# Kernel tuning notes

Measured on AMD Instinct MI355X. Metric: run time of the kernel, lower is better.

## Reference

```python
import jax, jax.numpy as jnp
import numpy as np

C_CURV = 1.0  # hyperbolic curvature (init kwarg c)
EPS = 1e-7


def _to_ball(v, max_norm=0.8):
    # rescale rows to lie strictly inside the unit Poincare ball
    n = jnp.linalg.norm(v, axis=-1, keepdims=True)
    return v * (max_norm / (n + 1.0))


def setup_inputs() -> dict:
    key = jax.random.key(0)
    k1, k2 = jax.random.split(key)
    B, C, D = 32768, 2048, 512
    z_mix = _to_ball(jax.random.normal(k1, (B, D), dtype=jnp.float32))
    prototypes = _to_ball(jax.random.normal(k2, (C, D), dtype=jnp.float32))
    repel_margin = jnp.float32(2.0)
    return {"z_mix": z_mix, "prototypes": prototypes, "repel_margin": repel_margin}


def dist_matrix(x, y, c):
    # Poincare-ball pairwise distance (arccosh form):
    # d(x,y) = arccosh(1 + 2c||x-y||^2 / ((1-c||x||^2)(1-c||y||^2))) / sqrt(c)
    x2 = jnp.sum(x * x, axis=-1)            # (B,)
    y2 = jnp.sum(y * y, axis=-1)            # (C,)
    xy = jnp.einsum('bd,cd->bc', x, y)      # (B, C)
    sqdist = jnp.maximum(x2[:, None] + y2[None, :] - 2.0 * xy, 0.0)
    denom = (1.0 - c * x2)[:, None] * (1.0 - c * y2)[None, :]
    arg = 1.0 + 2.0 * c * sqdist / jnp.maximum(denom, EPS)
    return jnp.arccosh(jnp.maximum(arg, 1.0 + EPS)) / jnp.sqrt(c)


def reference(z_mix, prototypes, repel_margin):
    dist2proto = dist_matrix(z_mix, prototypes, C_CURV)   # (B, C)
    min_dist = jnp.min(dist2proto, axis=1)                # (B,)
    return jnp.mean(jax.nn.relu(repel_margin - min_dist))
```

## Files before the change

kernel.cpp:

```cpp
#include <hip/hip_runtime.h>
#include <stdint.h>

#define EPS_F 1e-7f

typedef float f32x4 __attribute__((ext_vector_type(4)));

union A8 { uint2 u2; long l; };

__device__ __forceinline__ unsigned cvt4(float a, float b, float c, float d) {
  int v = __builtin_amdgcn_cvt_pk_fp8_f32(a, b, 0, false);
  return (unsigned)__builtin_amdgcn_cvt_pk_fp8_f32(c, d, v, true);
}

__global__ __launch_bounds__(256) void prep_kernel(
    const float* __restrict__ protos, uint8_t* __restrict__ wsB,
    float* __restrict__ y2a, float* __restrict__ rya,
    float* __restrict__ out) {
  const int lane = threadIdx.x & 63;
  const int w    = threadIdx.x >> 6;
  const int kp2  = lane >> 2, q = lane & 3;
  const int sl0  = 8 * kp2 + q;
  const int sl1  = sl0 + 4;
#pragma unroll
  for (int i = 0; i < 4; ++i) {
    int c = (blockIdx.x * 4 + w) * 4 + i;
    const float4* p = (const float4*)(protos + (size_t)c * 512 + lane * 8);
    float4 f0 = p[0], f1 = p[1];
    float s = f0.x*f0.x + f0.y*f0.y + f0.z*f0.z + f0.w*f0.w
            + f1.x*f1.x + f1.y*f1.y + f1.z*f1.z + f1.w*f1.w;
#pragma unroll
    for (int off = 32; off > 0; off >>= 1) s += __shfl_xor(s, off, 64);
    if (lane == 0) { y2a[c] = s; rya[c] = 1.f / (1.f - s); }
    unsigned ux = cvt4(f0.x, f0.y, f0.z, f0.w);
    unsigned uy = cvt4(f1.x, f1.y, f1.z, f1.w);
    uint4 ch;
    ch.x = __shfl((int)ux, sl0, 64);
    ch.y = __shfl((int)uy, sl0, 64);
    ch.z = __shfl((int)ux, sl1, 64);
    ch.w = __shfl((int)uy, sl1, 64);
    if (lane < 32) {
      int g = c >> 4, cl = c & 15;
      ((uint4*)wsB)[((size_t)g * 8 + kp2) * 64 + q * 16 + cl] = ch;
    }
  }
  if (blockIdx.x == 0 && threadIdx.x == 0) out[0] = 0.f;
}

__global__ __launch_bounds__(256, 2) void gemm_min_kernel(
    const float* __restrict__ z, const uint8_t* __restrict__ wsB,
    const float* __restrict__ y2a, const float* __restrict__ rya,
    const float* __restrict__ marg, float* __restrict__ out) {
  __shared__ uint8_t As[32 * 1024];
  __shared__ float x2s[64];
  __shared__ float rxs[64];
  __shared__ float minbuf[64][4];

  const int tid  = threadIdx.x;
  const int lane = tid & 63;
  const int w    = tid >> 6;
  const int q    = lane >> 4;
  const int l15  = lane & 15;
  const size_t rowbase = (size_t)blockIdx.x * 64;

  {
    const float* rp0 = z + (rowbase + w * 16 + l15) * 512;
    float s = 0.f;
#pragma unroll
    for (int j = 0; j < 8; ++j) {
      const float* rp = rp0 + j * 64 + q * 8;
      float4 a0 = ((const float4*)rp)[0];
      float4 a1 = ((const float4*)rp)[1];
      float4 b0 = ((const float4*)(rp + 32))[0];
      float4 b1 = ((const float4*)(rp + 32))[1];
      s += a0.x*a0.x + a0.y*a0.y + a0.z*a0.z + a0.w*a0.w
         + a1.x*a1.x + a1.y*a1.y + a1.z*a1.z + a1.w*a1.w
         + b0.x*b0.x + b0.y*b0.y + b0.z*b0.z + b0.w*b0.w
         + b1.x*b1.x + b1.y*b1.y + b1.z*b1.z + b1.w*b1.w;
      uint4 ch;
      ch.x = cvt4(a0.x, a0.y, a0.z, a0.w);
      ch.y = cvt4(a1.x, a1.y, a1.z, a1.w);
      ch.z = cvt4(b0.x, b0.y, b0.z, b0.w);
      ch.w = cvt4(b1.x, b1.y, b1.z, b1.w);
      ((uint4*)As)[(j * 4 + w) * 64 + lane] = ch;
    }
    s += __shfl_xor(s, 16, 64);
    s += __shfl_xor(s, 32, 64);
    if (lane < 16) { x2s[w * 16 + lane] = s; rxs[w * 16 + lane] = 1.f / (1.f - s); }
  }
  __syncthreads();

  float x2r[4][4];
#pragma unroll
  for (int rf = 0; rf < 4; ++rf) {
    float4 x4 = *(const float4*)&x2s[rf * 16 + q * 4];
    x2r[rf][0] = x4.x; x2r[rf][1] = x4.y; x2r[rf][2] = x4.z; x2r[rf][3] = x4.w;
  }

  const uint4* Ap = (const uint4*)As;
  const uint4* Bg = (const uint4*)wsB;

  uint4 B0w[4], B1w[4];
#pragma unroll
  for (int i = 0; i < 4; ++i) {
    B0w[i] = Bg[(size_t)(w * 256 + i) * 64 + lane];
    B1w[i] = Bg[(size_t)(w * 256 + 8 + i) * 64 + lane];
  }

  float tmin[4][4];
#pragma unroll
  for (int rf = 0; rf < 4; ++rf)
#pragma unroll
    for (int r = 0; r < 4; ++r) tmin[rf][r] = 3.4e38f;

  const float* y2p = y2a + w * 512 + l15;
  const float* ryp = rya + w * 512 + l15;

#pragma clang loop unroll(disable)
  for (int s = 0; s < 16; ++s) {
    f32x4 acc[4][2];
#pragma unroll
    for (int rf = 0; rf < 4; ++rf) {
      f32x4 z4 = {0.f, 0.f, 0.f, 0.f};
      acc[rf][0] = z4; acc[rf][1] = z4;
    }
    float y2v0 = y2p[s * 32],      ryv0 = ryp[s * 32];
    float y2v1 = y2p[s * 32 + 16], ryv1 = ryp[s * 32 + 16];

#pragma unroll
    for (int kp2 = 0; kp2 < 8; ++kp2) {
      uint4 bu0 = B0w[kp2 & 3];
      uint4 bu1 = B1w[kp2 & 3];
      {
        int ip = s * 8 + kp2 + 4;
        int sp = ip >> 3, kq = ip & 7;
        size_t c0 = (size_t)(w * 256 + sp * 16 + kq) * 64 + lane;
        B0w[kp2 & 3] = Bg[c0];
        B1w[kp2 & 3] = Bg[c0 + 8 * 64];
      }
      A8 b0lo, b0hi, b1lo, b1hi;
      b0lo.u2 = make_uint2(bu0.x, bu0.y); b0hi.u2 = make_uint2(bu0.z, bu0.w);
      b1lo.u2 = make_uint2(bu1.x, bu1.y); b1hi.u2 = make_uint2(bu1.z, bu1.w);
#pragma unroll
      for (int rf = 0; rf < 4; ++rf) {
        uint4 av = Ap[(kp2 * 4 + rf) * 64 + lane];
        A8 alo, ahi;
        alo.u2 = make_uint2(av.x, av.y);
        ahi.u2 = make_uint2(av.z, av.w);
        acc[rf][0] = __builtin_amdgcn_mfma_f32_16x16x32_fp8_fp8(
            alo.l, b0lo.l, acc[rf][0], 0, 0, 0);
        acc[rf][1] = __builtin_amdgcn_mfma_f32_16x16x32_fp8_fp8(
            alo.l, b1lo.l, acc[rf][1], 0, 0, 0);
        acc[rf][0] = __builtin_amdgcn_mfma_f32_16x16x32_fp8_fp8(
            ahi.l, b0hi.l, acc[rf][0], 0, 0, 0);
        acc[rf][1] = __builtin_amdgcn_mfma_f32_16x16x32_fp8_fp8(
            ahi.l, b1hi.l, acc[rf][1], 0, 0, 0);
      }
    }

#pragma unroll
    for (int rf = 0; rf < 4; ++rf) {
#pragma unroll
      for (int r = 0; r < 4; ++r) {
        float xv = x2r[rf][r];
        float u0 = fmaxf(fmaf(-2.f, acc[rf][0][r], xv + y2v0), 0.f) * ryv0;
        float u1 = fmaxf(fmaf(-2.f, acc[rf][1][r], xv + y2v1), 0.f) * ryv1;
        tmin[rf][r] = fminf(tmin[rf][r], fminf(u0, u1));
      }
    }
  }

#pragma unroll
  for (int rf = 0; rf < 4; ++rf) {
#pragma unroll
    for (int r = 0; r < 4; ++r) {
      float v = tmin[rf][r];
      v = fminf(v, __shfl_xor(v, 1, 64));
      v = fminf(v, __shfl_xor(v, 2, 64));
      v = fminf(v, __shfl_xor(v, 4, 64));
      v = fminf(v, __shfl_xor(v, 8, 64));
      if (l15 == 0) minbuf[rf * 16 + q * 4 + r][w] = v;
    }
  }
  __syncthreads();

  if (w == 0) {
    float m = fminf(fminf(minbuf[lane][0], minbuf[lane][1]),
                    fminf(minbuf[lane][2], minbuf[lane][3]));
    float t = m * rxs[lane];
    float arg = fmaxf(fmaf(2.f, t, 1.f), 1.f + EPS_F);
    float contrib = fmaxf(marg[0] - acoshf(arg), 0.f);
#pragma unroll
    for (int off = 32; off > 0; off >>= 1) contrib += __shfl_xor(contrib, off, 64);
    if (lane == 0) atomicAdd(out, contrib * (1.0f / 32768.f));
  }
}

extern "C" void kernel_launch(void* const* d_in, const int* in_sizes, int n_in,
                              void* d_out, int out_size, void* d_ws, size_t ws_size,
                              hipStream_t stream) {
  const float* z      = (const float*)d_in[0];
  const float* protos = (const float*)d_in[1];
  const float* marg   = (const float*)d_in[2];
  float* out = (float*)d_out;
  uint8_t* wsB = (uint8_t*)d_ws;
  float* y2a = (float*)((char*)d_ws + (1 << 20) + 192 * 1024);
  float* rya = y2a + 2048;

  prep_kernel<<<128, 256, 0, stream>>>(protos, wsB, y2a, rya, out);
  gemm_min_kernel<<<512, 256, 0, stream>>>(z, wsB, y2a, rya, marg, out);
}
```

Measured before the change: 155.9 us.

## Split prototype dimension across two blocks per row tile with atomic row-min

The GEMM-min kernel now launches 1024 blocks, with each row tile split into two halves of the prototype range. Partial row minima are merged with atomicMin on the float bits, and a new finish kernel applies acosh, the margin and the mean. The prep kernel is re-gridded to one prototype per wave and also initialises the row-min buffer. This doubles the grid to improve occupancy and tail balance on many CUs, at the cost of converting every z row tile to fp8 twice, an extra launch and extra global traffic.

```diff
diff --git a/kernel.cpp b/kernel.cpp
--- a/kernel.cpp
+++ b/kernel.cpp
@@ -15,44 +15,42 @@
 __global__ __launch_bounds__(256) void prep_kernel(
     const float* __restrict__ protos, uint8_t* __restrict__ wsB,
     float* __restrict__ y2a, float* __restrict__ rya,
-    float* __restrict__ out) {
+    unsigned* __restrict__ rowminU, float* __restrict__ out) {
   const int lane = threadIdx.x & 63;
   const int w    = threadIdx.x >> 6;
   const int kp2  = lane >> 2, q = lane & 3;
   const int sl0  = 8 * kp2 + q;
   const int sl1  = sl0 + 4;
-#pragma unroll
-  for (int i = 0; i < 4; ++i) {
-    int c = (blockIdx.x * 4 + w) * 4 + i;
-    const float4* p = (const float4*)(protos + (size_t)c * 512 + lane * 8);
-    float4 f0 = p[0], f1 = p[1];
-    float s = f0.x*f0.x + f0.y*f0.y + f0.z*f0.z + f0.w*f0.w
-            + f1.x*f1.x + f1.y*f1.y + f1.z*f1.z + f1.w*f1.w;
-#pragma unroll
-    for (int off = 32; off > 0; off >>= 1) s += __shfl_xor(s, off, 64);
-    if (lane == 0) { y2a[c] = s; rya[c] = 1.f / (1.f - s); }
-    unsigned ux = cvt4(f0.x, f0.y, f0.z, f0.w);
-    unsigned uy = cvt4(f1.x, f1.y, f1.z, f1.w);
-    uint4 ch;
-    ch.x = __shfl((int)ux, sl0, 64);
-    ch.y = __shfl((int)uy, sl0, 64);
-    ch.z = __shfl((int)ux, sl1, 64);
-    ch.w = __shfl((int)uy, sl1, 64);
-    if (lane < 32) {
-      int g = c >> 4, cl = c & 15;
-      ((uint4*)wsB)[((size_t)g * 8 + kp2) * 64 + q * 16 + cl] = ch;
-    }
-  }
-  if (blockIdx.x == 0 && threadIdx.x == 0) out[0] = 0.f;
+  const int c = blockIdx.x * 4 + w;
+  const float4* p = (const float4*)(protos + (size_t)c * 512 + lane * 8);
+  float4 f0 = p[0], f1 = p[1];
+  float s = f0.x*f0.x + f0.y*f0.y + f0.z*f0.z + f0.w*f0.w
+          + f1.x*f1.x + f1.y*f1.y + f1.z*f1.z + f1.w*f1.w;
+#pragma unroll
+  for (int off = 32; off > 0; off >>= 1) s += __shfl_xor(s, off, 64);
+  if (lane == 0) { y2a[c] = s; rya[c] = 1.f / (1.f - s); }
+  unsigned ux = cvt4(f0.x, f0.y, f0.z, f0.w);
+  unsigned uy = cvt4(f1.x, f1.y, f1.z, f1.w);
+  uint4 ch;
+  ch.x = __shfl((int)ux, sl0, 64);
+  ch.y = __shfl((int)uy, sl0, 64);
+  ch.z = __shfl((int)ux, sl1, 64);
+  ch.w = __shfl((int)uy, sl1, 64);
+  if (lane < 32) {
+    int g = c >> 4, cl = c & 15;
+    ((uint4*)wsB)[((size_t)g * 8 + kp2) * 64 + q * 16 + cl] = ch;
+  }
+  int tidg = blockIdx.x * 256 + threadIdx.x;
+  if (tidg < 32768) rowminU[tidg] = 0x7F7FFFFFu;
+  if (tidg == 0) out[0] = 0.f;
 }
 
 __global__ __launch_bounds__(256, 2) void gemm_min_kernel(
     const float* __restrict__ z, const uint8_t* __restrict__ wsB,
     const float* __restrict__ y2a, const float* __restrict__ rya,
-    const float* __restrict__ marg, float* __restrict__ out) {
+    float* __restrict__ rxa, unsigned* __restrict__ rowminU) {
   __shared__ uint8_t As[32 * 1024];
   __shared__ float x2s[64];
-  __shared__ float rxs[64];
   __shared__ float minbuf[64][4];
 
   const int tid  = threadIdx.x;
@@ -60,7 +58,19 @@
   const int w    = tid >> 6;
   const int q    = lane >> 4;
   const int l15  = lane & 15;
-  const size_t rowbase = (size_t)blockIdx.x * 64;
+  const int h    = blockIdx.x >> 9;
+  const int rt   = blockIdx.x & 511;
+  const size_t rowbase = (size_t)rt * 64;
+  const int bb   = h * 512 + w * 128;
+
+  const uint4* Bg = (const uint4*)wsB;
+
+  uint4 B0w[4], B1w[4];
+#pragma unroll
+  for (int i = 0; i < 4; ++i) {
+    B0w[i] = Bg[(size_t)(bb + i) * 64 + lane];
+    B1w[i] = Bg[(size_t)(bb + 8 + i) * 64 + lane];
+  }
 
   {
     const float* rp0 = z + (rowbase + w * 16 + l15) * 512;
@@ -85,7 +95,10 @@
     }
     s += __shfl_xor(s, 16, 64);
     s += __shfl_xor(s, 32, 64);
-    if (lane < 16) { x2s[w * 16 + lane] = s; rxs[w * 16 + lane] = 1.f / (1.f - s); }
+    if (lane < 16) {
+      x2s[w * 16 + lane] = s;
+      if (h == 0) rxa[rowbase + w * 16 + lane] = 1.f / (1.f - s);
+    }
   }
   __syncthreads();
 
@@ -97,14 +110,6 @@
   }
 
   const uint4* Ap = (const uint4*)As;
-  const uint4* Bg = (const uint4*)wsB;
-
-  uint4 B0w[4], B1w[4];
-#pragma unroll
-  for (int i = 0; i < 4; ++i) {
-    B0w[i] = Bg[(size_t)(w * 256 + i) * 64 + lane];
-    B1w[i] = Bg[(size_t)(w * 256 + 8 + i) * 64 + lane];
-  }
 
   float tmin[4][4];
 #pragma unroll
@@ -112,11 +117,11 @@
 #pragma unroll
     for (int r = 0; r < 4; ++r) tmin[rf][r] = 3.4e38f;
 
-  const float* y2p = y2a + w * 512 + l15;
-  const float* ryp = rya + w * 512 + l15;
+  const float* y2p = y2a + h * 1024 + w * 256 + l15;
+  const float* ryp = rya + h * 1024 + w * 256 + l15;
 
 #pragma clang loop unroll(disable)
-  for (int s = 0; s < 16; ++s) {
+  for (int s = 0; s < 8; ++s) {
     f32x4 acc[4][2];
 #pragma unroll
     for (int rf = 0; rf < 4; ++rf) {
@@ -133,7 +138,7 @@
       {
         int ip = s * 8 + kp2 + 4;
         int sp = ip >> 3, kq = ip & 7;
-        size_t c0 = (size_t)(w * 256 + sp * 16 + kq) * 64 + lane;
+        size_t c0 = (size_t)(bb + sp * 16 + kq) * 64 + lane;
         B0w[kp2 & 3] = Bg[c0];
         B1w[kp2 & 3] = Bg[c0 + 8 * 64];
       }
@@ -186,13 +191,22 @@
   if (w == 0) {
     float m = fminf(fminf(minbuf[lane][0], minbuf[lane][1]),
                     fminf(minbuf[lane][2], minbuf[lane][3]));
-    float t = m * rxs[lane];
-    float arg = fmaxf(fmaf(2.f, t, 1.f), 1.f + EPS_F);
-    float contrib = fmaxf(marg[0] - acoshf(arg), 0.f);
-#pragma unroll
-    for (int off = 32; off > 0; off >>= 1) contrib += __shfl_xor(contrib, off, 64);
-    if (lane == 0) atomicAdd(out, contrib * (1.0f / 32768.f));
-  }
+    atomicMin(&rowminU[rowbase + lane], __float_as_uint(m));
+  }
+}
+
+__global__ __launch_bounds__(256) void finish_kernel(
+    const unsigned* __restrict__ rowminU, const float* __restrict__ rxa,
+    const float* __restrict__ marg, float* __restrict__ out) {
+  const int row  = blockIdx.x * 256 + threadIdx.x;
+  const int lane = threadIdx.x & 63;
+  float m = __uint_as_float(rowminU[row]);
+  float t = m * rxa[row];
+  float arg = fmaxf(fmaf(2.f, t, 1.f), 1.f + EPS_F);
+  float contrib = fmaxf(marg[0] - acoshf(arg), 0.f);
+#pragma unroll
+  for (int off = 32; off > 0; off >>= 1) contrib += __shfl_xor(contrib, off, 64);
+  if (lane == 0) atomicAdd(out, contrib * (1.0f / 32768.f));
 }
 
 extern "C" void kernel_launch(void* const* d_in, const int* in_sizes, int n_in,
@@ -203,9 +217,13 @@
   const float* marg   = (const float*)d_in[2];
   float* out = (float*)d_out;
   uint8_t* wsB = (uint8_t*)d_ws;
-  float* y2a = (float*)((char*)d_ws + (1 << 20) + 192 * 1024);
-  float* rya = y2a + 2048;
-
-  prep_kernel<<<128, 256, 0, stream>>>(protos, wsB, y2a, rya, out);
-  gemm_min_kernel<<<512, 256, 0, stream>>>(z, wsB, y2a, rya, marg, out);
-}
+  char* base = (char*)d_ws + (1 << 20) + 192 * 1024;
+  float*    y2a     = (float*)base;
+  float*    rya     = y2a + 2048;
+  float*    rxa     = rya + 2048;
+  unsigned* rowminU = (unsigned*)(rxa + 32768);
+
+  prep_kernel<<<512, 256, 0, stream>>>(protos, wsB, y2a, rya, rowminU, out);
+  gemm_min_kernel<<<1024, 256, 0, stream>>>(z, wsB, y2a, rya, rxa, rowminU);
+  finish_kernel<<<128, 256, 0, stream>>>(rowminU, rxa, marg, out);
+}
```

Result: slower. 179.2 us (+14.9%).

## Switch FP8 GEMM to 16x16x128 scaled MFMA with re-laid-out operands

Applied to the files above, without the earlier changes.

Replaces the 16x16x32 FP8 MFMA with the gfx950 16x16x128 f8f6f4 scaled MFMA using unit scales. Both operand layouts change to match: prototype FP8 data is split into lo/hi halves in the workspace, and the activation tile in LDS is split into two arrays. The prep kernel now handles one prototype per wave, and the GEMM launch bound drops to one block per SIMD occupancy hint. The aim is fewer MFMA issues and more K per instruction, at the cost of register pressure from 8-dword operands and possibly lower occupancy.

```diff
diff --git a/kernel.cpp b/kernel.cpp
--- a/kernel.cpp
+++ b/kernel.cpp
@@ -4,13 +4,18 @@
 #define EPS_F 1e-7f
 
 typedef float f32x4 __attribute__((ext_vector_type(4)));
-
-union A8 { uint2 u2; long l; };
+typedef int   v8i   __attribute__((ext_vector_type(8)));
+
+union A32 { uint4 u4[2]; v8i v; };
 
 __device__ __forceinline__ unsigned cvt4(float a, float b, float c, float d) {
   int v = __builtin_amdgcn_cvt_pk_fp8_f32(a, b, 0, false);
   return (unsigned)__builtin_amdgcn_cvt_pk_fp8_f32(c, d, v, true);
 }
+
+#define MFMA128(A, B, C) __builtin_amdgcn_mfma_scale_f32_16x16x128_f8f6f4( \
+    (A), (B), (C), 0, 0, 0, 0x7F7F7F7F, 0, 0x7F7F7F7F)
+
 
 __global__ __launch_bounds__(256) void prep_kernel(
     const float* __restrict__ protos, uint8_t* __restrict__ wsB,
@@ -18,39 +23,30 @@
     float* __restrict__ out) {
   const int lane = threadIdx.x & 63;
   const int w    = threadIdx.x >> 6;
-  const int kp2  = lane >> 2, q = lane & 3;
-  const int sl0  = 8 * kp2 + q;
-  const int sl1  = sl0 + 4;
-#pragma unroll
-  for (int i = 0; i < 4; ++i) {
-    int c = (blockIdx.x * 4 + w) * 4 + i;
-    const float4* p = (const float4*)(protos + (size_t)c * 512 + lane * 8);
-    float4 f0 = p[0], f1 = p[1];
-    float s = f0.x*f0.x + f0.y*f0.y + f0.z*f0.z + f0.w*f0.w
-            + f1.x*f1.x + f1.y*f1.y + f1.z*f1.z + f1.w*f1.w;
-#pragma unroll
-    for (int off = 32; off > 0; off >>= 1) s += __shfl_xor(s, off, 64);
-    if (lane == 0) { y2a[c] = s; rya[c] = 1.f / (1.f - s); }
-    unsigned ux = cvt4(f0.x, f0.y, f0.z, f0.w);
-    unsigned uy = cvt4(f1.x, f1.y, f1.z, f1.w);
-    uint4 ch;
-    ch.x = __shfl((int)ux, sl0, 64);
-    ch.y = __shfl((int)uy, sl0, 64);
-    ch.z = __shfl((int)ux, sl1, 64);
-    ch.w = __shfl((int)uy, sl1, 64);
-    if (lane < 32) {
-      int g = c >> 4, cl = c & 15;
-      ((uint4*)wsB)[((size_t)g * 8 + kp2) * 64 + q * 16 + cl] = ch;
-    }
-  }
+  const int c    = blockIdx.x * 4 + w;
+  const int g    = c >> 4, cl = c & 15;
+  const float4* p = (const float4*)(protos + (size_t)c * 512 + lane * 8);
+  float4 f0 = p[0], f1 = p[1];
+  float s = f0.x*f0.x + f0.y*f0.y + f0.z*f0.z + f0.w*f0.w
+          + f1.x*f1.x + f1.y*f1.y + f1.z*f1.z + f1.w*f1.w;
+#pragma unroll
+  for (int off = 32; off > 0; off >>= 1) s += __shfl_xor(s, off, 64);
+  if (lane == 0) { y2a[c] = s; rya[c] = 1.f / (1.f - s); }
+  unsigned ux = cvt4(f0.x, f0.y, f0.z, f0.w);
+  unsigned uy = cvt4(f1.x, f1.y, f1.z, f1.w);
+  const int kb = lane >> 4, kg = (lane >> 2) & 3, bo = lane & 3;
+  size_t ri  = (size_t)(g * 4 + kb) * 64 + kg * 16 + cl;
+  size_t off = ri * 16 + (size_t)(bo & 1) * 8 + (size_t)(bo >> 1) * (512u * 1024u);
+  *(uint2*)(wsB + off) = make_uint2(ux, uy);
   if (blockIdx.x == 0 && threadIdx.x == 0) out[0] = 0.f;
 }
 
-__global__ __launch_bounds__(256, 2) void gemm_min_kernel(
+__global__ __launch_bounds__(256, 1) void gemm_min_kernel(
     const float* __restrict__ z, const uint8_t* __restrict__ wsB,
     const float* __restrict__ y2a, const float* __restrict__ rya,
     const float* __restrict__ marg, float* __restrict__ out) {
-  __shared__ uint8_t As[32 * 1024];
+  __shared__ uint4 AsLo[1024];
+  __shared__ uint4 AsHi[1024];
   __shared__ float x2s[64];
   __shared__ float rxs[64];
   __shared__ float minbuf[64][4];
@@ -62,26 +58,44 @@
   const int l15  = lane & 15;
   const size_t rowbase = (size_t)blockIdx.x * 64;
 
+  const uint4* BLo = (const uint4*)wsB;
+  const uint4* BHi = BLo + 32768;
+
+  A32 Bp0[4], Bp1[4];
+#pragma unroll
+  for (int i = 0; i < 4; ++i) {
+    size_t r0 = (size_t)(w * 128 + i) * 64 + lane;
+    Bp0[i].u4[0] = BLo[r0];       Bp0[i].u4[1] = BHi[r0];
+    Bp1[i].u4[0] = BLo[r0 + 256]; Bp1[i].u4[1] = BHi[r0 + 256];
+  }
+
   {
-    const float* rp0 = z + (rowbase + w * 16 + l15) * 512;
+    const float* rp0 = z + (rowbase + w * 16 + l15) * 512 + q * 128;
     float s = 0.f;
 #pragma unroll
-    for (int j = 0; j < 8; ++j) {
-      const float* rp = rp0 + j * 64 + q * 8;
-      float4 a0 = ((const float4*)rp)[0];
-      float4 a1 = ((const float4*)rp)[1];
-      float4 b0 = ((const float4*)(rp + 32))[0];
-      float4 b1 = ((const float4*)(rp + 32))[1];
-      s += a0.x*a0.x + a0.y*a0.y + a0.z*a0.z + a0.w*a0.w
-         + a1.x*a1.x + a1.y*a1.y + a1.z*a1.z + a1.w*a1.w
-         + b0.x*b0.x + b0.y*b0.y + b0.z*b0.z + b0.w*b0.w
-         + b1.x*b1.x + b1.y*b1.y + b1.z*b1.z + b1.w*b1.w;
-      uint4 ch;
-      ch.x = cvt4(a0.x, a0.y, a0.z, a0.w);
-      ch.y = cvt4(a1.x, a1.y, a1.z, a1.w);
-      ch.z = cvt4(b0.x, b0.y, b0.z, b0.w);
-      ch.w = cvt4(b1.x, b1.y, b1.z, b1.w);
-      ((uint4*)As)[(j * 4 + w) * 64 + lane] = ch;
+    for (int t = 0; t < 4; ++t) {
+      const float4* rp = (const float4*)(rp0 + t * 32);
+      float4 v0 = rp[0], v1 = rp[1], v2 = rp[2], v3 = rp[3];
+      float4 v4 = rp[4], v5 = rp[5], v6 = rp[6], v7 = rp[7];
+      s += v0.x*v0.x + v0.y*v0.y + v0.z*v0.z + v0.w*v0.w
+         + v1.x*v1.x + v1.y*v1.y + v1.z*v1.z + v1.w*v1.w
+         + v2.x*v2.x + v2.y*v2.y + v2.z*v2.z + v2.w*v2.w
+         + v3.x*v3.x + v3.y*v3.y + v3.z*v3.z + v3.w*v3.w
+         + v4.x*v4.x + v4.y*v4.y + v4.z*v4.z + v4.w*v4.w
+         + v5.x*v5.x + v5.y*v5.y + v5.z*v5.z + v5.w*v5.w
+         + v6.x*v6.x + v6.y*v6.y + v6.z*v6.z + v6.w*v6.w
+         + v7.x*v7.x + v7.y*v7.y + v7.z*v7.z + v7.w*v7.w;
+      uint4 lo, hi;
+      lo.x = cvt4(v0.x, v0.y, v0.z, v0.w);
+      lo.y = cvt4(v1.x, v1.y, v1.z, v1.w);
+      lo.z = cvt4(v2.x, v2.y, v2.z, v2.w);
+      lo.w = cvt4(v3.x, v3.y, v3.z, v3.w);
+      hi.x = cvt4(v4.x, v4.y, v4.z, v4.w);
+      hi.y = cvt4(v5.x, v5.y, v5.z, v5.w);
+      hi.z = cvt4(v6.x, v6.y, v6.z, v6.w);
+      hi.w = cvt4(v7.x, v7.y, v7.z, v7.w);
+      int ri = (q * 4 + w) * 64 + t * 16 + l15;
+      AsLo[ri] = lo; AsHi[ri] = hi;
     }
     s += __shfl_xor(s, 16, 64);
     s += __shfl_xor(s, 32, 64);
@@ -96,16 +110,6 @@
     x2r[rf][0] = x4.x; x2r[rf][1] = x4.y; x2r[rf][2] = x4.z; x2r[rf][3] = x4.w;
   }
 
-  const uint4* Ap = (const uint4*)As;
-  const uint4* Bg = (const uint4*)wsB;
-
-  uint4 B0w[4], B1w[4];
-#pragma unroll
-  for (int i = 0; i < 4; ++i) {
-    B0w[i] = Bg[(size_t)(w * 256 + i) * 64 + lane];
-    B1w[i] = Bg[(size_t)(w * 256 + 8 + i) * 64 + lane];
-  }
-
   float tmin[4][4];
 #pragma unroll
   for (int rf = 0; rf < 4; ++rf)
@@ -127,33 +131,22 @@
     float y2v1 = y2p[s * 32 + 16], ryv1 = ryp[s * 32 + 16];
 
 #pragma unroll
-    for (int kp2 = 0; kp2 < 8; ++kp2) {
-      uint4 bu0 = B0w[kp2 & 3];
-      uint4 bu1 = B1w[kp2 & 3];
+    for (int kb = 0; kb < 4; ++kb) {
+      v8i bv0 = Bp0[kb].v;
+      v8i bv1 = Bp1[kb].v;
       {
-        int ip = s * 8 + kp2 + 4;
-        int sp = ip >> 3, kq = ip & 7;
-        size_t c0 = (size_t)(w * 256 + sp * 16 + kq) * 64 + lane;
-        B0w[kp2 & 3] = Bg[c0];
-        B1w[kp2 & 3] = Bg[c0 + 8 * 64];
+        size_t r0 = ((size_t)(w * 32 + 2 * (s + 1)) * 4 + kb) * 64 + lane;
+        Bp0[kb].u4[0] = BLo[r0];       Bp0[kb].u4[1] = BHi[r0];
+        Bp1[kb].u4[0] = BLo[r0 + 256]; Bp1[kb].u4[1] = BHi[r0 + 256];
       }
-      A8 b0lo, b0hi, b1lo, b1hi;
-      b0lo.u2 = make_uint2(bu0.x, bu0.y); b0hi.u2 = make_uint2(bu0.z, bu0.w);
-      b1lo.u2 = make_uint2(bu1.x, bu1.y); b1hi.u2 = make_uint2(bu1.z, bu1.w);
 #pragma unroll
       for (int rf = 0; rf < 4; ++rf) {
-        uint4 av = Ap[(kp2 * 4 + rf) * 64 + lane];
-        A8 alo, ahi;
-        alo.u2 = make_uint2(av.x, av.y);
-        ahi.u2 = make_uint2(av.z, av.w);
-        acc[rf][0] = __builtin_amdgcn_mfma_f32_16x16x32_fp8_fp8(
-            alo.l, b0lo.l, acc[rf][0], 0, 0, 0);
-        acc[rf][1] = __builtin_amdgcn_mfma_f32_16x16x32_fp8_fp8(
-            alo.l, b1lo.l, acc[rf][1], 0, 0, 0);
-        acc[rf][0] = __builtin_amdgcn_mfma_f32_16x16x32_fp8_fp8(
-            ahi.l, b0hi.l, acc[rf][0], 0, 0, 0);
-        acc[rf][1] = __builtin_amdgcn_mfma_f32_16x16x32_fp8_fp8(
-            ahi.l, b1hi.l, acc[rf][1], 0, 0, 0);
+        A32 a;
+        int ri = (kb * 4 + rf) * 64 + lane;
+        a.u4[0] = AsLo[ri];
+        a.u4[1] = AsHi[ri];
+        acc[rf][0] = MFMA128(a.v, bv0, acc[rf][0]);
+        acc[rf][1] = MFMA128(a.v, bv1, acc[rf][1]);
       }
     }
 
@@ -206,6 +199,6 @@
   float* y2a = (float*)((char*)d_ws + (1 << 20) + 192 * 1024);
   float* rya = y2a + 2048;
 
-  prep_kernel<<<128, 256, 0, stream>>>(protos, wsB, y2a, rya, out);
+  prep_kernel<<<512, 256, 0, stream>>>(protos, wsB, y2a, rya, out);
   gemm_min_kernel<<<512, 256, 0, stream>>>(z, wsB, y2a, rya, marg, out);
 }
```

Result: faster. 147.1 us (-5.7%).
